# Performance work log

Hardware: AMD Instinct MI355X
Metric: run time of the kernel (lower is better)

Reference implementation:

```python
import jax, jax.numpy as jnp
import numpy as np

# slax LIF defaults
INIT_TAU = 2.0
BETA = jax.nn.sigmoid(INIT_TAU)  # membrane leak factor
VTH = 1.0                        # spike threshold
SLOPE = 25.0                     # fast-sigmoid surrogate slope

@jax.custom_vjp
def spike_fn(v):
    # heaviside forward, fast-sigmoid surrogate backward
    return (v >= 0.0).astype(v.dtype)

def _spike_fwd(v):
    return spike_fn(v), v

def _spike_bwd(v, g):
    return (g / (SLOPE * jnp.abs(v) + 1.0) ** 2,)

spike_fn.defvjp(_spike_fwd, _spike_bwd)


def setup_inputs() -> dict:
    key = jax.random.key(0)
    k1, k2 = jax.random.split(key, 2)
    B, T, F = 256, 2000, 128
    x = jax.random.normal(k1, (B, T, F), jnp.float32)
    # Dense(1) params (lecun_normal-ish init, zero bias)
    W = jax.random.normal(k2, (F, 1), jnp.float32) / jnp.sqrt(F)
    b = jnp.zeros((1,), jnp.float32)
    return {"x": x, "W": W, "b": b}


def reference(x, W, b):
    # Dense(1): [B,T,F] -> [B,T,1]
    cur = x @ W + b
    B = cur.shape[0]
    v0 = jnp.zeros((B, 1), cur.dtype)

    def step(v, c):
        v = BETA * v + c                  # leaky integrate
        s = spike_fn(v - VTH)             # threshold
        v = v - s * VTH                   # subtraction reset
        return v, s

    vT, spikes = jax.lax.scan(step, v0, jnp.swapaxes(cur, 0, 1))  # scan over time
    spikes = jnp.swapaxes(spikes, 0, 1)   # [B,T,1]
    return spikes, vT                     # (spike train, final Vmem)
```

## Files before the change

kernel.cpp:

```cpp
#include <hip/hip_runtime.h>

#define T_STEPS 2000
#define F_DIM   128
#define TILE    128
#define NTILES  16

__device__ __forceinline__ float group32_reduce(float p) {
#pragma unroll
  for (int m = 16; m >= 1; m >>= 1) p += __shfl_xor(p, m, 64);
  return p;
}

__global__ __launch_bounds__(256, 1) void lif_fused(
    const float* __restrict__ x, const float* __restrict__ W,
    const float* __restrict__ bias, float* __restrict__ out, int B) {
  const float BETA = 0.8807970779778823f;
  const float VTH  = 1.0f;

  const int b      = blockIdx.x;
  const int tid    = threadIdx.x;
  const int lane   = tid & 63;
  const int wave   = tid >> 6;
  const int fgrp   = tid & 31;
  const int rowoff = tid >> 5;

  __shared__ float curbuf[2][TILE];

  const float4* xb = (const float4*)(x + (size_t)b * T_STEPS * F_DIM);
  const float4  w4 = ((const float4*)W)[fgrp];
  const float   bs = bias[0];
  float* outb = out + (size_t)b * T_STEPS;

  float4 xv[16];
  float  v = 0.0f;

  auto load_tile = [&](int c) {
    const int base = c * TILE;
#pragma unroll
    for (int r = 0; r < 16; ++r) {
      const int row = base + r * 8 + rowoff;
      if (row < T_STEPS) xv[r] = xb[row * 32 + fgrp];
      else               xv[r] = make_float4(0.f, 0.f, 0.f, 0.f);
    }
  };

  auto reduce_tile = [&](int c) {
    const int base = c * TILE;
    float* wb = curbuf[c & 1];
#pragma unroll
    for (int r = 0; r < 16; ++r) {
      float p = xv[r].x * w4.x;
      p = fmaf(xv[r].y, w4.y, p);
      p = fmaf(xv[r].z, w4.z, p);
      p = fmaf(xv[r].w, w4.w, p);
      p = group32_reduce(p);
      if (fgrp == 0) {
        const int row = base + r * 8 + rowoff;
        if (row < T_STEPS) wb[r * 8 + rowoff] = p + bs;
      }
    }
  };

  load_tile(0);
  reduce_tile(0);
  __syncthreads();

  for (int c = 0; c < NTILES; ++c) {
    if (c + 1 < NTILES) load_tile(c + 1);

    if (wave == 0) {
      const float* cb   = curbuf[c & 1];
      const int    base = c * TILE;
      const int    tlen = (T_STEPS - base < TILE) ? (T_STEPS - base) : TILE;
      float sp0 = 0.f, sp1 = 0.f;
      float cv[32], cn[32];
#pragma unroll
      for (int q = 0; q < 8; ++q)
        *(float4*)&cv[q * 4] = *(const float4*)&cb[q * 4];

      if (tlen == TILE) {
#pragma unroll
        for (int g = 0; g < 4; ++g) {
          if (g < 3) {
#pragma unroll
            for (int q = 0; q < 8; ++q)
              *(float4*)&cn[q * 4] = *(const float4*)&cb[(g + 1) * 32 + q * 4];
          }
#pragma unroll
          for (int j = 0; j < 32; ++j) {
            const int t = g * 32 + j;
            v = __fadd_rn(__fmul_rn(BETA, v), cv[j]);
            const float d = v - VTH;
            const float s = (d >= 0.f) ? 1.f : 0.f;
            v = (d >= 0.f) ? d : v;
            if (lane == (t & 63)) { if (t < 64) sp0 = s; else sp1 = s; }
          }
          if (g < 3) {
#pragma unroll
            for (int j = 0; j < 32; ++j) cv[j] = cn[j];
          }
        }
      } else {
#pragma unroll
        for (int g = 0; g < 4; ++g) {
          if (g * 32 < tlen) {
            if (g > 0) {
#pragma unroll
              for (int q = 0; q < 8; ++q)
                *(float4*)&cv[q * 4] = *(const float4*)&cb[g * 32 + q * 4];
            }
#pragma unroll
            for (int j = 0; j < 32; ++j) {
              const int  t     = g * 32 + j;
              const bool valid = (t < tlen);
              float vn = __fadd_rn(__fmul_rn(BETA, v), cv[j]);
              const float d = vn - VTH;
              const float s = (d >= 0.f) ? 1.f : 0.f;
              vn = (d >= 0.f) ? d : vn;
              if (valid) {
                v = vn;
                if (lane == (t & 63)) { if (t < 64) sp0 = s; else sp1 = s; }
              }
            }
          }
        }
      }
      if (lane < tlen)      outb[base + lane]      = sp0;
      if (64 + lane < tlen) outb[base + 64 + lane] = sp1;
    }

    if (c + 1 < NTILES) reduce_tile(c + 1);
    __syncthreads();
  }

  if (tid == 0) out[(size_t)B * T_STEPS + b] = v;
}

extern "C" void kernel_launch(void* const* d_in, const int* in_sizes, int n_in,
                              void* d_out, int out_size, void* d_ws, size_t ws_size,
                              hipStream_t stream) {
  const float* x    = (const float*)d_in[0];
  const float* W    = (const float*)d_in[1];
  const float* bias = (const float*)d_in[2];
  float* out = (float*)d_out;
  const int B = in_sizes[0] / (T_STEPS * F_DIM);
  lif_fused<<<dim3(B), dim3(256), 0, stream>>>(x, W, bias, out, B);
}
```

Baseline: 370.8 us.

## Split into grid-wide dense reduction kernel and batch-parallel LIF scan kernel

Replaces the fused per-batch kernel with two kernels. The first is a grid-stride dense projection that writes currents transposed to [T,B] in workspace. The second runs the time scan with one lane per batch element (4 blocks of 64), staging spikes through padded shared memory for coalesced writes. This removes the serial single-wave scan that kept only one block per batch busy. The cost is a workspace round trip, an extra launch, and a scan phase that uses only 4 wavefronts on the whole GPU.

Result: slower. 460.0 us (+24.1%).

```diff
diff --git a/kernel.cpp b/kernel.cpp
--- a/kernel.cpp
+++ b/kernel.cpp
@@ -1,139 +1,119 @@
 #include <hip/hip_runtime.h>
 
+#define B_DIM   256
 #define T_STEPS 2000
 #define F_DIM   128
-#define TILE    128
-#define NTILES  16
+#define N_ROWS  (B_DIM * T_STEPS)
+#define N_GRP   (N_ROWS / 4)
 
-__device__ __forceinline__ float group32_reduce(float p) {
-#pragma unroll
-  for (int m = 16; m >= 1; m >>= 1) p += __shfl_xor(p, m, 64);
-  return p;
+__global__ __launch_bounds__(256) void dense_rows(
+    const float* __restrict__ x, const float* __restrict__ W,
+    const float* __restrict__ bias, float* __restrict__ curT) {
+  const int tid    = threadIdx.x;
+  const int lane   = tid & 63;
+  const int sub    = lane & 15;
+  const int grp    = lane >> 4;
+  const int waveId = (blockIdx.x * 256 + tid) >> 6;
+  const int nWaves = gridDim.x * 4;
+
+  const float4 wlo = ((const float4*)W)[sub];
+  const float4 whi = ((const float4*)W)[sub + 16];
+  const float  bs  = bias[0];
+
+  for (int g = waveId; g < N_GRP; g += nWaves) {
+    const int rid0 = g * 4;
+    const int b    = rid0 / T_STEPS;
+    const int t0   = rid0 - b * T_STEPS;
+    const int rid  = rid0 + grp;
+
+    const float4* row = (const float4*)(x + (size_t)rid * F_DIM);
+    const float4  xl  = row[sub];
+    const float4  xh  = row[sub + 16];
+
+    float pl = xl.x * wlo.x;
+    pl = fmaf(xl.y, wlo.y, pl);
+    pl = fmaf(xl.z, wlo.z, pl);
+    pl = fmaf(xl.w, wlo.w, pl);
+    float ph = xh.x * whi.x;
+    ph = fmaf(xh.y, whi.y, ph);
+    ph = fmaf(xh.z, whi.z, ph);
+    ph = fmaf(xh.w, whi.w, ph);
+
+    float s = pl + ph;
+    s += __shfl_xor(s, 8, 64);
+    s += __shfl_xor(s, 4, 64);
+    s += __shfl_xor(s, 2, 64);
+    s += __shfl_xor(s, 1, 64);
+
+    if (sub == 0) curT[(t0 + grp) * B_DIM + b] = s + bs;
+  }
 }
 
-__global__ __launch_bounds__(256, 1) void lif_fused(
-    const float* __restrict__ x, const float* __restrict__ W,
-    const float* __restrict__ bias, float* __restrict__ out, int B) {
+__global__ __launch_bounds__(64) void lif_scan(
+    const float* __restrict__ curT, float* __restrict__ out) {
   const float BETA = 0.8807970779778823f;
   const float VTH  = 1.0f;
 
-  const int b      = blockIdx.x;
-  const int tid    = threadIdx.x;
-  const int lane   = tid & 63;
-  const int wave   = tid >> 6;
-  const int fgrp   = tid & 31;
-  const int rowoff = tid >> 5;
+  __shared__ float sb[64 * 65];
+  const int lane = threadIdx.x;
+  const int boff = blockIdx.x * 64;
+  const int gb   = boff + lane;
 
-  __shared__ float curbuf[2][TILE];
+  float v = 0.0f;
+  float cv[64], cn[64];
 
-  const float4* xb = (const float4*)(x + (size_t)b * T_STEPS * F_DIM);
-  const float4  w4 = ((const float4*)W)[fgrp];
-  const float   bs = bias[0];
-  float* outb = out + (size_t)b * T_STEPS;
+#pragma unroll
+  for (int j = 0; j < 64; ++j) cv[j] = curT[j * B_DIM + gb];
 
-  float4 xv[16];
-  float  v = 0.0f;
-
-  auto load_tile = [&](int c) {
-    const int base = c * TILE;
+  for (int k = 0; k < 32; ++k) {
+    if (k < 31) {
+      const int tbase = (k + 1) * 64;
 #pragma unroll
-    for (int r = 0; r < 16; ++r) {
-      const int row = base + r * 8 + rowoff;
-      if (row < T_STEPS) xv[r] = xb[row * 32 + fgrp];
-      else               xv[r] = make_float4(0.f, 0.f, 0.f, 0.f);
-    }
-  };
-
-  auto reduce_tile = [&](int c) {
-    const int base = c * TILE;
-    float* wb = curbuf[c & 1];
-#pragma unroll
-    for (int r = 0; r < 16; ++r) {
-      float p = xv[r].x * w4.x;
-      p = fmaf(xv[r].y, w4.y, p);
-      p = fmaf(xv[r].z, w4.z, p);
-      p = fmaf(xv[r].w, w4.w, p);
-      p = group32_reduce(p);
-      if (fgrp == 0) {
-        const int row = base + r * 8 + rowoff;
-        if (row < T_STEPS) wb[r * 8 + rowoff] = p + bs;
+      for (int j = 0; j < 64; ++j) {
+        const int tn = tbase + j;
+        cn[j] = (tn < T_STEPS) ? curT[tn * B_DIM + gb] : 0.0f;
       }
     }
-  };
 
-  load_tile(0);
-  reduce_tile(0);
-  __syncthreads();
+    const int t0  = k * 64;
+    const int len = (T_STEPS - t0 < 64) ? (T_STEPS - t0) : 64;
 
-  for (int c = 0; c < NTILES; ++c) {
-    if (c + 1 < NTILES) load_tile(c + 1);
+    if (len == 64) {
+#pragma unroll
+      for (int j = 0; j < 64; ++j) {
+        v = __fadd_rn(__fmul_rn(BETA, v), cv[j]);
+        const float d = v - VTH;
+        const float s = (d >= 0.0f) ? 1.0f : 0.0f;
+        v = (d >= 0.0f) ? d : v;
+        sb[lane * 65 + j] = s;
+      }
+    } else {
+#pragma unroll
+      for (int j = 0; j < 16; ++j) {
+        v = __fadd_rn(__fmul_rn(BETA, v), cv[j]);
+        const float d = v - VTH;
+        const float s = (d >= 0.0f) ? 1.0f : 0.0f;
+        v = (d >= 0.0f) ? d : v;
+        sb[lane * 65 + j] = s;
+      }
+    }
+    __syncthreads();
 
-    if (wave == 0) {
-      const float* cb   = curbuf[c & 1];
-      const int    base = c * TILE;
-      const int    tlen = (T_STEPS - base < TILE) ? (T_STEPS - base) : TILE;
-      float sp0 = 0.f, sp1 = 0.f;
-      float cv[32], cn[32];
+    if (t0 + lane < T_STEPS) {
+#pragma unroll 8
+      for (int r = 0; r < 64; ++r) {
+        out[(size_t)(boff + r) * T_STEPS + t0 + lane] = sb[r * 65 + lane];
+      }
+    }
+    __syncthreads();
+
+    if (k < 31) {
 #pragma unroll
-      for (int q = 0; q < 8; ++q)
-        *(float4*)&cv[q * 4] = *(const float4*)&cb[q * 4];
-
-      if (tlen == TILE) {
-#pragma unroll
-        for (int g = 0; g < 4; ++g) {
-          if (g < 3) {
-#pragma unroll
-            for (int q = 0; q < 8; ++q)
-              *(float4*)&cn[q * 4] = *(const float4*)&cb[(g + 1) * 32 + q * 4];
-          }
-#pragma unroll
-          for (int j = 0; j < 32; ++j) {
-            const int t = g * 32 + j;
-            v = __fadd_rn(__fmul_rn(BETA, v), cv[j]);
-            const float d = v - VTH;
-            const float s = (d >= 0.f) ? 1.f : 0.f;
-            v = (d >= 0.f) ? d : v;
-            if (lane == (t & 63)) { if (t < 64) sp0 = s; else sp1 = s; }
-          }
-          if (g < 3) {
-#pragma unroll
-            for (int j = 0; j < 32; ++j) cv[j] = cn[j];
-          }
-        }
-      } else {
-#pragma unroll
-        for (int g = 0; g < 4; ++g) {
-          if (g * 32 < tlen) {
-            if (g > 0) {
-#pragma unroll
-              for (int q = 0; q < 8; ++q)
-                *(float4*)&cv[q * 4] = *(const float4*)&cb[g * 32 + q * 4];
-            }
-#pragma unroll
-            for (int j = 0; j < 32; ++j) {
-              const int  t     = g * 32 + j;
-              const bool valid = (t < tlen);
-              float vn = __fadd_rn(__fmul_rn(BETA, v), cv[j]);
-              const float d = vn - VTH;
-              const float s = (d >= 0.f) ? 1.f : 0.f;
-              vn = (d >= 0.f) ? d : vn;
-              if (valid) {
-                v = vn;
-                if (lane == (t & 63)) { if (t < 64) sp0 = s; else sp1 = s; }
-              }
-            }
-          }
-        }
-      }
-      if (lane < tlen)      outb[base + lane]      = sp0;
-      if (64 + lane < tlen) outb[base + 64 + lane] = sp1;
+      for (int j = 0; j < 64; ++j) cv[j] = cn[j];
     }
-
-    if (c + 1 < NTILES) reduce_tile(c + 1);
-    __syncthreads();
   }
 
-  if (tid == 0) out[(size_t)B * T_STEPS + b] = v;
+  out[(size_t)B_DIM * T_STEPS + gb] = v;
 }
 
 extern "C" void kernel_launch(void* const* d_in, const int* in_sizes, int n_in,
@@ -142,7 +122,9 @@
   const float* x    = (const float*)d_in[0];
   const float* W    = (const float*)d_in[1];
   const float* bias = (const float*)d_in[2];
-  float* out = (float*)d_out;
-  const int B = in_sizes[0] / (T_STEPS * F_DIM);
-  lif_fused<<<dim3(B), dim3(256), 0, stream>>>(x, W, bias, out, B);
+  float* out  = (float*)d_out;
+  float* curT = (float*)d_ws;
+
+  dense_rows<<<dim3(2048), dim3(256), 0, stream>>>(x, W, bias, curT);
+  lif_scan<<<dim3(B_DIM / 64), dim3(64), 0, stream>>>(curT, out);
 }
```
